# Kernel optimization log

Hardware: AMD Instinct MI355X
Metric: run time of the kernel (lower is better)

The kernel has to match this reference:

```python
import jax, jax.numpy as jnp
import numpy as np

N_USER = 60000
N_ITEM = 40000
N = N_USER + N_ITEM          # 100000 nodes
D = 64                       # embed / layer dim
NNZ = 1600000                # edges per relation (avg degree 16)
B = 16384                    # batch of (user,item) pairs
NLAYERS = 2                  # layers=[64,64,64] -> 2 GNN layers
VAL_SCALE = 0.02             # ~1/degree, mimics symmetric-normalized Laplacian values
W_SCALE = 0.05


def spmm(row, col, val, X):
    # sparse [N,N] @ dense [N,D] via gather + segment-sum (COO)
    return jax.ops.segment_sum(val[:, None] * X[col], row, num_segments=N)


def setup_inputs() -> dict:
    key = jax.random.key(0)
    ks = jax.random.split(key, 40)
    inp = {}
    inp['userIdx'] = jax.random.randint(ks[0], (B,), 0, N_USER, dtype=jnp.int32)
    inp['itemIdx'] = jax.random.randint(ks[1], (B,), 0, N_ITEM, dtype=jnp.int32)
    inp['uEmbd'] = jax.random.normal(ks[2], (N_USER, D), dtype=jnp.float32)
    inp['iEmbd'] = jax.random.normal(ks[3], (N_ITEM, D), dtype=jnp.float32)
    for i, name in enumerate(['lap', 'trust', 'add']):
        inp[name + '_row'] = jax.random.randint(ks[4 + 3 * i], (NNZ,), 0, N, dtype=jnp.int32)
        inp[name + '_col'] = jax.random.randint(ks[5 + 3 * i], (NNZ,), 0, N, dtype=jnp.int32)
        inp[name + '_val'] = jax.random.uniform(ks[6 + 3 * i], (NNZ,), dtype=jnp.float32) * VAL_SCALE
    j = 13
    for name in ['lin_W', 'inter_W', 'attM_W', 'attA_W', 'attT_W']:
        inp[name] = jax.random.normal(ks[j], (NLAYERS, D, D), dtype=jnp.float32) * W_SCALE; j += 1
    for name in ['lin_b', 'inter_b', 'attM_b', 'attA_b', 'attT_b']:
        inp[name] = jax.random.normal(ks[j], (NLAYERS, D), dtype=jnp.float32) * W_SCALE; j += 1
    for name in ['a_main', 'a_add', 'a_trust']:
        inp[name] = jax.random.normal(ks[j], (NLAYERS, D, 1), dtype=jnp.float32) * W_SCALE; j += 1
    inp['W1'] = jax.random.normal(ks[j], (2 * D, 64), dtype=jnp.float32) * W_SCALE; j += 1
    inp['b1'] = jax.random.normal(ks[j], (64,), dtype=jnp.float32) * W_SCALE; j += 1
    inp['W2'] = jax.random.normal(ks[j], (64, 32), dtype=jnp.float32) * W_SCALE; j += 1
    inp['b2'] = jax.random.normal(ks[j], (32,), dtype=jnp.float32) * W_SCALE; j += 1
    inp['W3'] = jax.random.normal(ks[j], (32, 1), dtype=jnp.float32) * W_SCALE; j += 1
    inp['b3'] = jax.random.normal(ks[j], (1,), dtype=jnp.float32) * W_SCALE; j += 1
    return inp


def _gcf_forward(userIdx, itemIdx, uEmbd, iEmbd,
                 lap_row, lap_col, lap_val,
                 trust_row, trust_col, trust_val,
                 add_row, add_col, add_val,
                 lin_W, lin_b, inter_W, inter_b,
                 attM_W, attM_b, attA_W, attA_b, attT_W, attT_b,
                 a_main, a_add, a_trust,
                 W1, b1, W2, b2, W3, b3):
    feats = jnp.concatenate([uEmbd, iEmbd], axis=0)  # [N, D]
    all_emb = [feats]
    rels = [(lap_row, lap_col, lap_val),
            (trust_row, trust_col, trust_val),
            (add_row, add_col, add_val)]
    for l in range(NLAYERS):
        X = feats
        X2 = X * X  # inter_feature = features * features

        def relation(edges, aW, ab, avec):
            row, col, val = edges
            # (L + I) @ X  -> linear ; L @ (X*X) -> interActTransform
            h1 = (spmm(row, col, val, X) + X) @ lin_W[l] + lin_b[l]
            h2 = spmm(row, col, val, X2) @ inter_W[l] + inter_b[l]
            att = jnp.tanh((h1 + h2) @ aW + ab) @ avec  # [N, 1]
            return h1, h2, att.mean()

        m1, m2, w_main = relation(rels[0], attM_W[l], attM_b[l], a_main[l])
        t1, t2, w_trust = relation(rels[1], attT_W[l], attT_b[l], a_trust[l])
        a1, a2, w_add = relation(rels[2], attA_W[l], attA_b[l], a_add[l])
        beta = jax.nn.softmax(jnp.stack([w_main, w_add, w_trust]))  # [3]
        feats = (beta[0] * (m1 + m2) + beta[1] * (a1 + a2) + beta[2] * (t1 + t2))
        all_emb.append(feats)
    final = jnp.mean(jnp.stack(all_emb, axis=1), axis=1)  # [N, D]
    userE = final[userIdx]
    itemE = final[itemIdx + N_USER]
    h = jnp.concatenate([userE, itemE], axis=1)  # [B, 2D]
    h = jax.nn.relu(h @ W1 + b1)
    h = h @ W2 + b2
    h = h @ W3 + b3
    prediction = h.reshape(-1)
    return prediction, userE, itemE, final


def reference(userIdx, itemIdx, uEmbd, iEmbd,
              lap_row, lap_col, lap_val,
              trust_row, trust_col, trust_val,
              add_row, add_col, add_val,
              lin_W, lin_b, inter_W, inter_b,
              attM_W, attM_b, attA_W, attA_b, attT_W, attT_b,
              a_main, a_add, a_trust,
              W1, b1, W2, b2, W3, b3):
    return _gcf_forward(userIdx, itemIdx, uEmbd, iEmbd,
                        lap_row, lap_col, lap_val,
                        trust_row, trust_col, trust_val,
                        add_row, add_col, add_val,
                        lin_W, lin_b, inter_W, inter_b,
                        attM_W, attM_b, attA_W, attA_b, attT_W, attT_b,
                        a_main, a_add, a_trust,
                        W1, b1, W2, b2, W3, b3)
```

## Files before the change

### kernel.cpp

```cpp
#include <hip/hip_runtime.h>

#define N_USER  60000
#define N_ITEM  40000
#define NN      100000
#define NNZ_E   1600000
#define BB      16384
#define ND      6400000
#define ND4     1600000
#define NCHUNK  6250
#define NBUCK   196
#define BUCK_CAP 9216
#define BUCKTOT (NBUCK * BUCK_CAP)
#define BINB    196
#define EPB     8192

typedef __attribute__((ext_vector_type(8))) short bf16x8;
typedef __attribute__((ext_vector_type(4))) float f32x4;

__device__ __forceinline__ float tanh_fast(float x) {
    x = fminf(fmaxf(x, -15.f), 15.f);
    float e = __expf(2.f * x);
    return (e - 1.f) / (e + 1.f);
}

__device__ __forceinline__ float bcast(float x, int k) {
    return __int_as_float(__builtin_amdgcn_readlane(__float_as_int(x), k));
}

__device__ __forceinline__ unsigned short f2bf(float f) {
    unsigned u = __float_as_uint(f);
    u += 0x7FFFu + ((u >> 16) & 1u);
    return (unsigned short)(u >> 16);
}
__device__ __forceinline__ float bf2f(unsigned short s) {
    return __uint_as_float(((unsigned)s) << 16);
}

__device__ __forceinline__ int widx(int k, int n) {
    return ((((n >> 4) * 2 + (k >> 5)) * 4 + ((k >> 3) & 3)) * 16 + (n & 15)) * 8 + (k & 7);
}

__global__ __launch_bounds__(256) void init_kernel(
    const float4* __restrict__ u, const float4* __restrict__ it,
    ushort* __restrict__ XB, float4* __restrict__ fs,
    int* __restrict__ CURS, float* __restrict__ attsum)
{
    int i = blockIdx.x * 256 + threadIdx.x;
    if (i < ND4) {
        float4 v = (i < N_USER * 16) ? u[i] : it[i - N_USER * 16];
        fs[i] = v;
        ushort4 b;
        b.x = f2bf(v.x); b.y = f2bf(v.y); b.z = f2bf(v.z); b.w = f2bf(v.w);
        ((ushort4*)XB)[i] = b;
    }
    if (i < 3 * NBUCK) CURS[i] = (i % NBUCK) * BUCK_CAP;
    if (i < 6) attsum[i] = 0.f;
}

__global__ __launch_bounds__(256) void bin_kernel(
    const int* __restrict__ rows0, const int* __restrict__ cols0, const float* __restrict__ vals0,
    const int* __restrict__ rows1, const int* __restrict__ cols1, const float* __restrict__ vals1,
    const int* __restrict__ rows2, const int* __restrict__ cols2, const float* __restrict__ vals2,
    int* __restrict__ CURS, int2* __restrict__ ECV)
{
    int rel = blockIdx.x / BINB;
    int blk = blockIdx.x % BINB;
    const int* rows; const int* cols; const float* vals;
    if (rel == 0) { rows = rows0; cols = cols0; vals = vals0; }
    else if (rel == 1) { rows = rows1; cols = cols1; vals = vals1; }
    else { rows = rows2; cols = cols2; vals = vals2; }
    int2* out = ECV + (size_t)rel * BUCKTOT;

    __shared__ int2 sStage[EPB];
    __shared__ int hW[4 * NBUCK];
    __shared__ int lOff[NBUCK], lEnd[NBUCK], lCur[NBUCK], gB[NBUCK];
    __shared__ int wt[4];

    int t = threadIdx.x;
    int lane = t & 63, w = t >> 6;
    for (int i = t; i < 4 * NBUCK; i += 256) hW[i] = 0;
    __syncthreads();

    int base = blk * EPB;
    #pragma unroll
    for (int j = 0; j < EPB / 256; ++j) {
        int idx = base + j * 256 + t;
        if (idx < NNZ_E) atomicAdd(&hW[w * NBUCK + (rows[idx] >> 9)], 1);
    }
    __syncthreads();
    int h = 0;
    if (t < NBUCK)
        h = hW[t] + hW[NBUCK + t] + hW[2 * NBUCK + t] + hW[3 * NBUCK + t];
    int sc = h;
    #pragma unroll
    for (int o = 1; o < 64; o <<= 1) {
        int u = __shfl_up(sc, o);
        if (lane >= o) sc += u;
    }
    if (lane == 63) wt[w] = sc;
    __syncthreads();
    int woff = 0;
    #pragma unroll
    for (int ww = 0; ww < 4; ++ww) if (ww < w) woff += wt[ww];
    int excl = woff + sc - h;
    if (t < NBUCK) {
        lOff[t] = excl;
        lEnd[t] = excl + h;
        lCur[t] = excl;
        gB[t] = h ? atomicAdd(&CURS[rel * NBUCK + t], h) : 0;
    }
    __syncthreads();
    #pragma unroll
    for (int j = 0; j < EPB / 256; ++j) {
        int idx = base + j * 256 + t;
        if (idx < NNZ_E) {
            int r = rows[idx];
            int b = r >> 9;
            int pos = atomicAdd(&lCur[b], 1);
            int2 e;
            e.x = ((r & 511) << 17) | cols[idx];
            e.y = __float_as_int(vals[idx]);
            sStage[pos] = e;
        }
    }
    __syncthreads();
    for (int b = w; b < NBUCK; b += 4) {
        int s = lOff[b], e = lEnd[b];
        int gb = gB[b];
        int lim = (b + 1) * BUCK_CAP;
        for (int i = s + lane; i < e; i += 64) {
            int d = gb + (i - s);
            if (d < lim) out[d] = sStage[i];
        }
    }
}

__global__ __launch_bounds__(256) void bsort_kernel(
    const int* __restrict__ CURS, int2* __restrict__ ECV,
    int* __restrict__ RPS, int* __restrict__ RPE)
{
    int rel = blockIdx.x / NBUCK;
    int b   = blockIdx.x % NBUCK;
    int start = b * BUCK_CAP;
    int cnt = CURS[rel * NBUCK + b] - start;
    if (cnt > BUCK_CAP) cnt = BUCK_CAP;
    int2* ecv = ECV + (size_t)rel * BUCKTOT;

    __shared__ int2 sStage[BUCK_CAP];
    __shared__ int sOff[512], sCur[512];
    __shared__ int wt[4];
    int t = threadIdx.x;
    sCur[2 * t] = 0; sCur[2 * t + 1] = 0;
    __syncthreads();
    for (int i = t; i < cnt; i += 256) {
        int rl = ((unsigned)ecv[start + i].x) >> 17;
        atomicAdd(&sCur[rl], 1);
    }
    __syncthreads();
    int a0 = sCur[2 * t], a1 = sCur[2 * t + 1];
    int ps = a0 + a1;
    int lane = t & 63, w = t >> 6;
    int sc = ps;
    #pragma unroll
    for (int o = 1; o < 64; o <<= 1) {
        int u = __shfl_up(sc, o);
        if (lane >= o) sc += u;
    }
    if (lane == 63) wt[w] = sc;
    __syncthreads();
    int woff = 0;
    #pragma unroll
    for (int ww = 0; ww < 4; ++ww) if (ww < w) woff += wt[ww];
    int excl = woff + sc - ps;
    __syncthreads();
    sOff[2 * t] = excl;
    sOff[2 * t + 1] = excl + a0;
    sCur[2 * t] = excl;
    sCur[2 * t + 1] = excl + a0;
    __syncthreads();
    for (int i = t; i < cnt; i += 256) {
        int2 e = ecv[start + i];
        int rl = ((unsigned)e.x) >> 17;
        int pos = atomicAdd(&sCur[rl], 1);
        int2 o2; o2.x = e.x & 0x1FFFF; o2.y = e.y;
        sStage[pos] = o2;
    }
    __syncthreads();
    for (int i = t; i < cnt; i += 256) ecv[start + i] = sStage[i];
    #pragma unroll
    for (int j = 0; j < 2; ++j) {
        int i = 2 * t + j;
        int row = b * 512 + i;
        if (row < NN) {
            RPS[rel * NN + row] = start + sOff[i];
            RPE[rel * NN + row] = start + sCur[i];
        }
    }
}

__global__ __launch_bounds__(256, 8) void spmm_kernel(
    const int* __restrict__ RPS, const int* __restrict__ RPE,
    const int2* __restrict__ ecv,
    const ushort* __restrict__ XB, ushort* __restrict__ G)
{
    int t = threadIdx.x;
    int lane = t & 63;
    int wv = t >> 6;
    int dl = lane & 15;
    int r = blockIdx.x * 16 + wv * 4 + (lane >> 4);
    int ea = RPS[r], eb = RPE[r];
    int cnt = eb - ea;
    int cm = cnt;
    cm = max(cm, __shfl_xor(cm, 16));
    cm = max(cm, __shfl_xor(cm, 32));
    ushort4 xo4 = *(const ushort4*)&XB[(size_t)r * 64 + 4 * dl];
    float s1[4] = {0.f, 0.f, 0.f, 0.f};
    float s2[4] = {0.f, 0.f, 0.f, 0.f};
    for (int base = 0; base < cm; base += 8) {
        float vv[8]; ushort4 xx[8];
        #pragma unroll
        for (int j = 0; j < 8; ++j) {
            int i = base + j;
            bool ok = i < cnt;
            int is = ea + (ok ? i : 0);
            int2 cv = ecv[is];
            vv[j] = ok ? __int_as_float(cv.y) : 0.f;
            xx[j] = *(const ushort4*)&XB[(size_t)cv.x * 64 + 4 * dl];
        }
        #pragma unroll
        for (int j = 0; j < 8; ++j) {
            float x0 = bf2f(xx[j].x), x1 = bf2f(xx[j].y);
            float x2 = bf2f(xx[j].z), x3 = bf2f(xx[j].w);
            float v = vv[j];
            s1[0] += v * x0; s2[0] += v * x0 * x0;
            s1[1] += v * x1; s2[1] += v * x1 * x1;
            s1[2] += v * x2; s2[2] += v * x2 * x2;
            s1[3] += v * x3; s2[3] += v * x3 * x3;
        }
    }
    ushort4 o1, o2;
    o1.x = f2bf(s1[0] + bf2f(xo4.x)); o1.y = f2bf(s1[1] + bf2f(xo4.y));
    o1.z = f2bf(s1[2] + bf2f(xo4.z)); o1.w = f2bf(s1[3] + bf2f(xo4.w));
    o2.x = f2bf(s2[0]); o2.y = f2bf(s2[1]); o2.z = f2bf(s2[2]); o2.w = f2bf(s2[3]);
    *(ushort4*)&G[(size_t)r * 128 + 4 * dl]      = o1;
    *(ushort4*)&G[(size_t)r * 128 + 64 + 4 * dl] = o2;
}

__global__ __launch_bounds__(256) void dense_kernel(
    const ushort* __restrict__ G, ushort* __restrict__ Hout,
    const float* __restrict__ linW, const float* __restrict__ interW,
    const float* __restrict__ linb, const float* __restrict__ interb,
    const float* __restrict__ attW, const float* __restrict__ attb,
    const float* __restrict__ avec, float* __restrict__ attsum)
{
    __shared__ short sL[4096], sI[4096], sW[4096];
    __shared__ float sH[4 * 16 * 65];
    __shared__ float sBias[64], sAttb[64], sAvec[64];

    int tid = threadIdx.x;
    for (int i = tid; i < 4096; i += 256) {
        int k = i >> 6, n = i & 63, ix = widx(k, n);
        sL[ix] = (short)f2bf(linW[i]);
        sI[ix] = (short)f2bf(interW[i]);
        sW[ix] = (short)f2bf(attW[i]);
    }
    if (tid < 64) {
        sBias[tid] = linb[tid] + interb[tid];
        sAttb[tid] = attb[tid];
        sAvec[tid] = avec[tid];
    }
    __syncthreads();

    const bf16x8* pL = (const bf16x8*)sL;
    const bf16x8* pI = (const bf16x8*)sI;
    const bf16x8* pW = (const bf16x8*)sW;

    int lane = tid & 63;
    int wv = tid >> 6;
    int nl = lane & 15;
    int q  = lane >> 4;
    float* myH = sH + wv * (16 * 65);
    int gw = blockIdx.x * 4 + wv;
    int nw = gridDim.x * 4;
    float att_acc = 0.f;

    for (int c = gw; c < NCHUNK; c += nw) {
        int r0 = c * 16;
        const bf16x8* gp = (const bf16x8*)(G + (size_t)(r0 + nl) * 128);
        bf16x8 Ah[2], Qh[2];
        Ah[0] = gp[q];         Ah[1] = gp[4 + q];
        Qh[0] = gp[8 + q];     Qh[1] = gp[12 + q];
        #pragma unroll
        for (int nt = 0; nt < 4; ++nt) {
            float b = sBias[nt * 16 + nl];
            f32x4 acc = {b, b, b, b};
            #pragma unroll
            for (int kh = 0; kh < 2; ++kh) {
                int f = ((nt * 2 + kh) * 4 + q) * 16 + nl;
                acc = __builtin_amdgcn_mfma_f32_16x16x32_bf16(Ah[kh], pL[f], acc, 0, 0, 0);
                acc = __builtin_amdgcn_mfma_f32_16x16x32_bf16(Qh[kh], pI[f], acc, 0, 0, 0);
            }
            #pragma unroll
            for (int reg = 0; reg < 4; ++reg) {
                int row = q * 4 + reg;
                Hout[(size_t)(r0 + row) * 64 + nt * 16 + nl] = f2bf(acc[reg]);
                myH[row * 65 + nt * 16 + nl] = acc[reg];
            }
        }
        bf16x8 Th[2];
        #pragma unroll
        for (int kh = 0; kh < 2; ++kh) {
            #pragma unroll
            for (int j = 0; j < 8; ++j)
                Th[kh][j] = (short)f2bf(myH[nl * 65 + kh * 32 + q * 8 + j]);
        }
        #pragma unroll
        for (int nt = 0; nt < 4; ++nt) {
            float b = sAttb[nt * 16 + nl];
            f32x4 acc = {b, b, b, b};
            #pragma unroll
            for (int kh = 0; kh < 2; ++kh) {
                int f = ((nt * 2 + kh) * 4 + q) * 16 + nl;
                acc = __builtin_amdgcn_mfma_f32_16x16x32_bf16(Th[kh], pW[f], acc, 0, 0, 0);
            }
            float av = sAvec[nt * 16 + nl];
            #pragma unroll
            for (int reg = 0; reg < 4; ++reg)
                att_acc += tanh_fast(acc[reg]) * av;
        }
    }
    #pragma unroll
    for (int o = 32; o >= 1; o >>= 1) att_acc += __shfl_xor(att_acc, o);
    if (lane == 0) atomicAdd(attsum, att_acc);
}

__global__ __launch_bounds__(256) void combine_kernel(
    const ushort4* __restrict__ hM, const ushort4* __restrict__ hA,
    const ushort4* __restrict__ hT, const float* __restrict__ attsum,
    ushort4* __restrict__ XB, float4* __restrict__ fs, float scale)
{
    float w0 = attsum[0] * (1.f / NN);
    float w1 = attsum[1] * (1.f / NN);
    float w2 = attsum[2] * (1.f / NN);
    float m = fmaxf(w0, fmaxf(w1, w2));
    float e0 = __expf(w0 - m), e1 = __expf(w1 - m), e2 = __expf(w2 - m);
    float inv = 1.f / (e0 + e1 + e2);
    float b0 = e0 * inv, b1 = e1 * inv, b2 = e2 * inv;

    int i = blockIdx.x * 256 + threadIdx.x;
    if (i >= ND4) return;
    ushort4 um = hM[i], ua = hA[i], ut = hT[i];
    float4 x;
    x.x = b0 * bf2f(um.x) + b1 * bf2f(ua.x) + b2 * bf2f(ut.x);
    x.y = b0 * bf2f(um.y) + b1 * bf2f(ua.y) + b2 * bf2f(ut.y);
    x.z = b0 * bf2f(um.z) + b1 * bf2f(ua.z) + b2 * bf2f(ut.z);
    x.w = b0 * bf2f(um.w) + b1 * bf2f(ua.w) + b2 * bf2f(ut.w);
    ushort4 bo;
    bo.x = f2bf(x.x); bo.y = f2bf(x.y); bo.z = f2bf(x.z); bo.w = f2bf(x.w);
    XB[i] = bo;
    float4 f = fs[i];
    f.x = (f.x + x.x) * scale;
    f.y = (f.y + x.y) * scale;
    f.z = (f.z + x.z) * scale;
    f.w = (f.w + x.w) * scale;
    fs[i] = f;
}

__global__ __launch_bounds__(256) void mlp_kernel(
    const int* __restrict__ userIdx, const int* __restrict__ itemIdx,
    const float* __restrict__ fin,
    const float* __restrict__ W1, const float* __restrict__ b1,
    const float* __restrict__ W2, const float* __restrict__ b2,
    const float* __restrict__ W3, const float* __restrict__ b3,
    float* __restrict__ pred, float* __restrict__ userE, float* __restrict__ itemE)
{
    __shared__ float sW1[128 * 64];
    __shared__ float sW2[64 * 32];
    __shared__ float sW3[32];
    __shared__ float sb1[64];
    __shared__ float sb2[32];
    int tid = threadIdx.x;
    for (int i = tid; i < 8192; i += 256) sW1[i] = W1[i];
    for (int i = tid; i < 2048; i += 256) sW2[i] = W2[i];
    if (tid < 32) sW3[tid] = W3[tid];
    if (tid < 64) sb1[tid] = b1[tid];
    if (tid < 32) sb2[tid] = b2[tid];
    __syncthreads();
    float bb3 = b3[0];

    int lane = tid & 63;
    int gw = blockIdx.x * 4 + (tid >> 6);
    int nw = gridDim.x * 4;
    for (int p = gw; p < BB; p += nw) {
        int u = userIdx[p];
        int it = itemIdx[p] + N_USER;
        float ue = fin[u * 64 + lane];
        float ie = fin[it * 64 + lane];
        userE[p * 64 + lane] = ue;
        itemE[p * 64 + lane] = ie;
        float h = sb1[lane];
        #pragma unroll
        for (int k = 0; k < 64; ++k) h = fmaf(bcast(ue, k), sW1[k * 64 + lane], h);
        #pragma unroll
        for (int k = 0; k < 64; ++k) h = fmaf(bcast(ie, k), sW1[(k + 64) * 64 + lane], h);
        h = fmaxf(h, 0.f);
        float h2 = sb2[lane & 31];
        #pragma unroll
        for (int k = 0; k < 64; ++k) h2 = fmaf(bcast(h, k), sW2[k * 32 + (lane & 31)], h2);
        float c = (lane < 32) ? h2 * sW3[lane] : 0.f;
        #pragma unroll
        for (int o = 32; o >= 1; o >>= 1) c += __shfl_xor(c, o);
        if (lane == 0) pred[p] = c + bb3;
    }
}

extern "C" void kernel_launch(void* const* d_in, const int* in_sizes, int n_in,
                              void* d_out, int out_size, void* d_ws, size_t ws_size,
                              hipStream_t stream)
{
    const int*   userIdx = (const int*)d_in[0];
    const int*   itemIdx = (const int*)d_in[1];
    const float* uEmbd   = (const float*)d_in[2];
    const float* iEmbd   = (const float*)d_in[3];
    const int*   e_row[3] = {(const int*)d_in[4],  (const int*)d_in[10], (const int*)d_in[7]};
    const int*   e_col[3] = {(const int*)d_in[5],  (const int*)d_in[11], (const int*)d_in[8]};
    const float* e_val[3] = {(const float*)d_in[6], (const float*)d_in[12], (const float*)d_in[9]};
    const float* lin_W   = (const float*)d_in[13];
    const float* inter_W = (const float*)d_in[14];
    const float* attM_W  = (const float*)d_in[15];
    const float* attA_W  = (const float*)d_in[16];
    const float* attT_W  = (const float*)d_in[17];
    const float* lin_b   = (const float*)d_in[18];
    const float* inter_b = (const float*)d_in[19];
    const float* attM_b  = (const float*)d_in[20];
    const float* attA_b  = (const float*)d_in[21];
    const float* attT_b  = (const float*)d_in[22];
    const float* a_main  = (const float*)d_in[23];
    const float* a_add   = (const float*)d_in[24];
    const float* a_trust = (const float*)d_in[25];
    const float* W1 = (const float*)d_in[26];
    const float* b1 = (const float*)d_in[27];
    const float* W2 = (const float*)d_in[28];
    const float* b2 = (const float*)d_in[29];
    const float* W3 = (const float*)d_in[30];
    const float* b3 = (const float*)d_in[31];

    const float* attWq[3] = {attM_W, attA_W, attT_W};
    const float* attbq[3] = {attM_b, attA_b, attT_b};
    const float* avecq[3] = {a_main, a_add, a_trust};

    ushort* G  = (ushort*)d_ws;
    ushort* H0 = G + (size_t)NN * 128;
    ushort* H1 = H0 + ND;
    ushort* H2 = H1 + ND;
    int2*   ECV = (int2*)(H2 + ND);
    ushort* XB = (ushort*)(ECV + 3 * (size_t)BUCKTOT);
    int*    RPS = (int*)(XB + ND);
    int*    RPE = RPS + 3 * NN;
    int*    CURS = RPE + 3 * NN;
    float*  ATT = (float*)(CURS + 3 * NBUCK);

    ushort* Hs[3] = {H0, H1, H2};

    float* outPred  = (float*)d_out;
    float* outUser  = outPred + BB;
    float* outItem  = outUser + BB * 64;
    float* outFinal = outItem + BB * 64;

    init_kernel<<<6250, 256, 0, stream>>>((const float4*)uEmbd, (const float4*)iEmbd,
                                          XB, (float4*)outFinal, CURS, ATT);
    bin_kernel<<<3 * BINB, 256, 0, stream>>>(
        e_row[0], e_col[0], e_val[0],
        e_row[1], e_col[1], e_val[1],
        e_row[2], e_col[2], e_val[2], CURS, ECV);
    bsort_kernel<<<3 * NBUCK, 256, 0, stream>>>(CURS, ECV, RPS, RPE);

    for (int l = 0; l < 2; ++l) {
        const float* lw = lin_W + l * 4096;
        const float* iw = inter_W + l * 4096;
        const float* lb = lin_b + l * 64;
        const float* ib = inter_b + l * 64;

        for (int q = 0; q < 3; ++q) {
            spmm_kernel<<<6250, 256, 0, stream>>>(
                RPS + q * NN, RPE + q * NN, ECV + (size_t)q * BUCKTOT, XB, G);
            dense_kernel<<<512, 256, 0, stream>>>(
                G, Hs[q], lw, iw, lb, ib,
                attWq[q] + l * 4096, attbq[q] + l * 64, avecq[q] + l * 64,
                ATT + l * 3 + q);
        }
        combine_kernel<<<6250, 256, 0, stream>>>(
            (const ushort4*)Hs[0], (const ushort4*)Hs[1], (const ushort4*)Hs[2],
            ATT + l * 3, (ushort4*)XB, (float4*)outFinal,
            (l == 1) ? (1.f / 3.f) : 1.f);
    }

    mlp_kernel<<<512, 256, 0, stream>>>(userIdx, itemIdx, outFinal,
                                        W1, b1, W2, b2, W3, b3,
                                        outPred, outUser, outItem);
}
```

Before: 932.0 us.

## Widen SpMM gathers to 16-byte loads and cache edges in registers during binning

SpMM now gives each row 8 lanes instead of 16. Each lane gathers 8 bf16 features with one 16-byte load, and the unroll depth drops from 8 to 4 edges. The bin and bucket-sort kernels move to 512 threads. They keep row indices and edges in registers so global memory is not read twice, and they use nontemporal loads and stores for the streaming edge data. The aim is fewer, wider memory instructions and less redundant edge traffic. The costs are fewer outstanding gathers per lane, higher register pressure, and a barrier placed inside a divergent branch in the bin kernel.

```diff
diff --git a/kernel.cpp b/kernel.cpp
--- a/kernel.cpp
+++ b/kernel.cpp
@@ -15,6 +15,7 @@
 #define EPB     8192
 
 typedef __attribute__((ext_vector_type(8))) short bf16x8;
+typedef __attribute__((ext_vector_type(8))) unsigned short u16x8;
 typedef __attribute__((ext_vector_type(4))) float f32x4;
 
 __device__ __forceinline__ float tanh_fast(float x) {
@@ -57,7 +58,7 @@
     if (i < 6) attsum[i] = 0.f;
 }
 
-__global__ __launch_bounds__(256) void bin_kernel(
+__global__ __launch_bounds__(512) void bin_kernel(
     const int* __restrict__ rows0, const int* __restrict__ cols0, const float* __restrict__ vals0,
     const int* __restrict__ rows1, const int* __restrict__ cols1, const float* __restrict__ vals1,
     const int* __restrict__ rows2, const int* __restrict__ cols2, const float* __restrict__ vals2,
@@ -69,73 +70,86 @@
     if (rel == 0) { rows = rows0; cols = cols0; vals = vals0; }
     else if (rel == 1) { rows = rows1; cols = cols1; vals = vals1; }
     else { rows = rows2; cols = cols2; vals = vals2; }
-    int2* out = ECV + (size_t)rel * BUCKTOT;
+    long long* out = (long long*)(ECV + (size_t)rel * BUCKTOT);
 
     __shared__ int2 sStage[EPB];
-    __shared__ int hW[4 * NBUCK];
+    __shared__ int hW[8 * NBUCK];
     __shared__ int lOff[NBUCK], lEnd[NBUCK], lCur[NBUCK], gB[NBUCK];
     __shared__ int wt[4];
 
     int t = threadIdx.x;
     int lane = t & 63, w = t >> 6;
-    for (int i = t; i < 4 * NBUCK; i += 256) hW[i] = 0;
+    for (int i = t; i < 8 * NBUCK; i += 512) hW[i] = 0;
     __syncthreads();
 
     int base = blk * EPB;
-    #pragma unroll
-    for (int j = 0; j < EPB / 256; ++j) {
-        int idx = base + j * 256 + t;
-        if (idx < NNZ_E) atomicAdd(&hW[w * NBUCK + (rows[idx] >> 9)], 1);
-    }
-    __syncthreads();
-    int h = 0;
-    if (t < NBUCK)
-        h = hW[t] + hW[NBUCK + t] + hW[2 * NBUCK + t] + hW[3 * NBUCK + t];
-    int sc = h;
-    #pragma unroll
-    for (int o = 1; o < 64; o <<= 1) {
-        int u = __shfl_up(sc, o);
-        if (lane >= o) sc += u;
-    }
-    if (lane == 63) wt[w] = sc;
-    __syncthreads();
-    int woff = 0;
-    #pragma unroll
-    for (int ww = 0; ww < 4; ++ww) if (ww < w) woff += wt[ww];
-    int excl = woff + sc - h;
-    if (t < NBUCK) {
-        lOff[t] = excl;
-        lEnd[t] = excl + h;
-        lCur[t] = excl;
-        gB[t] = h ? atomicAdd(&CURS[rel * NBUCK + t], h) : 0;
-    }
-    __syncthreads();
-    #pragma unroll
-    for (int j = 0; j < EPB / 256; ++j) {
-        int idx = base + j * 256 + t;
-        if (idx < NNZ_E) {
-            int r = rows[idx];
-            int b = r >> 9;
+    int myrow[16];
+    #pragma unroll
+    for (int j = 0; j < 16; ++j) {
+        int idx = base + j * 512 + t;
+        myrow[j] = (idx < NNZ_E) ? __builtin_nontemporal_load(&rows[idx]) : -1;
+        if (myrow[j] >= 0) atomicAdd(&hW[w * NBUCK + (myrow[j] >> 9)], 1);
+    }
+    __syncthreads();
+    if (t < 256) {
+        int h = 0;
+        if (t < NBUCK) {
+            #pragma unroll
+            for (int ww = 0; ww < 8; ++ww) h += hW[ww * NBUCK + t];
+        }
+        int sc = h;
+        #pragma unroll
+        for (int o = 1; o < 64; o <<= 1) {
+            int u = __shfl_up(sc, o);
+            if (lane >= o) sc += u;
+        }
+        if (lane == 63) wt[w] = sc;
+        __syncthreads();
+        int woff = 0;
+        #pragma unroll
+        for (int ww = 0; ww < 4; ++ww) if (ww < w) woff += wt[ww];
+        int excl = woff + sc - h;
+        if (t < NBUCK) {
+            lOff[t] = excl;
+            lEnd[t] = excl + h;
+            lCur[t] = excl;
+            gB[t] = h ? atomicAdd(&CURS[rel * NBUCK + t], h) : 0;
+        }
+    } else {
+        __syncthreads();
+    }
+    __syncthreads();
+    #pragma unroll
+    for (int j = 0; j < 16; ++j) {
+        int idx = base + j * 512 + t;
+        if (myrow[j] >= 0) {
+            int c = __builtin_nontemporal_load(&cols[idx]);
+            float v = __builtin_nontemporal_load(&vals[idx]);
+            int b = myrow[j] >> 9;
             int pos = atomicAdd(&lCur[b], 1);
             int2 e;
-            e.x = ((r & 511) << 17) | cols[idx];
-            e.y = __float_as_int(vals[idx]);
+            e.x = ((myrow[j] & 511) << 17) | c;
+            e.y = __float_as_int(v);
             sStage[pos] = e;
         }
     }
     __syncthreads();
-    for (int b = w; b < NBUCK; b += 4) {
+    for (int b = w; b < NBUCK; b += 8) {
         int s = lOff[b], e = lEnd[b];
         int gb = gB[b];
         int lim = (b + 1) * BUCK_CAP;
         for (int i = s + lane; i < e; i += 64) {
             int d = gb + (i - s);
-            if (d < lim) out[d] = sStage[i];
-        }
-    }
-}
-
-__global__ __launch_bounds__(256) void bsort_kernel(
+            if (d < lim) {
+                int2 ev = sStage[i];
+                long long packed = (((long long)(unsigned)ev.y) << 32) | (unsigned)ev.x;
+                __builtin_nontemporal_store(packed, &out[d]);
+            }
+        }
+    }
+}
+
+__global__ __launch_bounds__(512) void bsort_kernel(
     const int* __restrict__ CURS, int2* __restrict__ ECV,
     int* __restrict__ RPS, int* __restrict__ RPE)
 {
@@ -147,20 +161,24 @@
     int2* ecv = ECV + (size_t)rel * BUCKTOT;
 
     __shared__ int2 sStage[BUCK_CAP];
-    __shared__ int sOff[512], sCur[512];
-    __shared__ int wt[4];
+    __shared__ int sOff[512], sCnt[512];
+    __shared__ int wt[8];
     int t = threadIdx.x;
-    sCur[2 * t] = 0; sCur[2 * t + 1] = 0;
-    __syncthreads();
-    for (int i = t; i < cnt; i += 256) {
-        int rl = ((unsigned)ecv[start + i].x) >> 17;
-        atomicAdd(&sCur[rl], 1);
-    }
-    __syncthreads();
-    int a0 = sCur[2 * t], a1 = sCur[2 * t + 1];
-    int ps = a0 + a1;
     int lane = t & 63, w = t >> 6;
-    int sc = ps;
+    sCnt[t] = 0;
+    __syncthreads();
+    int2 e[18];
+    #pragma unroll
+    for (int j = 0; j < 18; ++j) {
+        int i = t + j * 512;
+        if (i < cnt) {
+            e[j] = ecv[start + i];
+            atomicAdd(&sCnt[((unsigned)e[j].x) >> 17], 1);
+        }
+    }
+    __syncthreads();
+    int h = sCnt[t];
+    int sc = h;
     #pragma unroll
     for (int o = 1; o < 64; o <<= 1) {
         int u = __shfl_up(sc, o);
@@ -170,35 +188,32 @@
     __syncthreads();
     int woff = 0;
     #pragma unroll
-    for (int ww = 0; ww < 4; ++ww) if (ww < w) woff += wt[ww];
-    int excl = woff + sc - ps;
-    __syncthreads();
-    sOff[2 * t] = excl;
-    sOff[2 * t + 1] = excl + a0;
-    sCur[2 * t] = excl;
-    sCur[2 * t + 1] = excl + a0;
-    __syncthreads();
-    for (int i = t; i < cnt; i += 256) {
-        int2 e = ecv[start + i];
-        int rl = ((unsigned)e.x) >> 17;
-        int pos = atomicAdd(&sCur[rl], 1);
-        int2 o2; o2.x = e.x & 0x1FFFF; o2.y = e.y;
-        sStage[pos] = o2;
-    }
-    __syncthreads();
-    for (int i = t; i < cnt; i += 256) ecv[start + i] = sStage[i];
-    #pragma unroll
-    for (int j = 0; j < 2; ++j) {
-        int i = 2 * t + j;
-        int row = b * 512 + i;
-        if (row < NN) {
-            RPS[rel * NN + row] = start + sOff[i];
-            RPE[rel * NN + row] = start + sCur[i];
-        }
-    }
-}
-
-__global__ __launch_bounds__(256, 8) void spmm_kernel(
+    for (int ww = 0; ww < 8; ++ww) if (ww < w) woff += wt[ww];
+    int excl = woff + sc - h;
+    __syncthreads();
+    sOff[t] = excl;
+    sCnt[t] = excl;
+    __syncthreads();
+    #pragma unroll
+    for (int j = 0; j < 18; ++j) {
+        int i = t + j * 512;
+        if (i < cnt) {
+            int rl = ((unsigned)e[j].x) >> 17;
+            int pos = atomicAdd(&sCnt[rl], 1);
+            int2 o2; o2.x = e[j].x & 0x1FFFF; o2.y = e[j].y;
+            sStage[pos] = o2;
+        }
+    }
+    __syncthreads();
+    for (int i = t; i < cnt; i += 512) ecv[start + i] = sStage[i];
+    int row = b * 512 + t;
+    if (row < NN) {
+        RPS[rel * NN + row] = start + sOff[t];
+        RPE[rel * NN + row] = start + sCnt[t];
+    }
+}
+
+__global__ __launch_bounds__(256, 4) void spmm_kernel(
     const int* __restrict__ RPS, const int* __restrict__ RPE,
     const int2* __restrict__ ecv,
     const ushort* __restrict__ XB, ushort* __restrict__ G)
@@ -206,44 +221,47 @@
     int t = threadIdx.x;
     int lane = t & 63;
     int wv = t >> 6;
-    int dl = lane & 15;
-    int r = blockIdx.x * 16 + wv * 4 + (lane >> 4);
+    int dl = lane & 7;
+    int r = blockIdx.x * 32 + wv * 8 + (lane >> 3);
     int ea = RPS[r], eb = RPE[r];
     int cnt = eb - ea;
     int cm = cnt;
+    cm = max(cm, __shfl_xor(cm, 8));
     cm = max(cm, __shfl_xor(cm, 16));
     cm = max(cm, __shfl_xor(cm, 32));
-    ushort4 xo4 = *(const ushort4*)&XB[(size_t)r * 64 + 4 * dl];
-    float s1[4] = {0.f, 0.f, 0.f, 0.f};
-    float s2[4] = {0.f, 0.f, 0.f, 0.f};
-    for (int base = 0; base < cm; base += 8) {
-        float vv[8]; ushort4 xx[8];
-        #pragma unroll
-        for (int j = 0; j < 8; ++j) {
+    u16x8 xo8 = *(const u16x8*)&XB[(size_t)r * 64 + 8 * dl];
+    float s1[8] = {0.f, 0.f, 0.f, 0.f, 0.f, 0.f, 0.f, 0.f};
+    float s2[8] = {0.f, 0.f, 0.f, 0.f, 0.f, 0.f, 0.f, 0.f};
+    for (int base = 0; base < cm; base += 4) {
+        float vv[4]; u16x8 xx[4];
+        #pragma unroll
+        for (int j = 0; j < 4; ++j) {
             int i = base + j;
             bool ok = i < cnt;
             int is = ea + (ok ? i : 0);
             int2 cv = ecv[is];
             vv[j] = ok ? __int_as_float(cv.y) : 0.f;
-            xx[j] = *(const ushort4*)&XB[(size_t)cv.x * 64 + 4 * dl];
-        }
-        #pragma unroll
-        for (int j = 0; j < 8; ++j) {
-            float x0 = bf2f(xx[j].x), x1 = bf2f(xx[j].y);
-            float x2 = bf2f(xx[j].z), x3 = bf2f(xx[j].w);
+            xx[j] = *(const u16x8*)&XB[(size_t)cv.x * 64 + 8 * dl];
+        }
+        #pragma unroll
+        for (int j = 0; j < 4; ++j) {
             float v = vv[j];
-            s1[0] += v * x0; s2[0] += v * x0 * x0;
-            s1[1] += v * x1; s2[1] += v * x1 * x1;
-            s1[2] += v * x2; s2[2] += v * x2 * x2;
-            s1[3] += v * x3; s2[3] += v * x3 * x3;
-        }
-    }
-    ushort4 o1, o2;
-    o1.x = f2bf(s1[0] + bf2f(xo4.x)); o1.y = f2bf(s1[1] + bf2f(xo4.y));
-    o1.z = f2bf(s1[2] + bf2f(xo4.z)); o1.w = f2bf(s1[3] + bf2f(xo4.w));
-    o2.x = f2bf(s2[0]); o2.y = f2bf(s2[1]); o2.z = f2bf(s2[2]); o2.w = f2bf(s2[3]);
-    *(ushort4*)&G[(size_t)r * 128 + 4 * dl]      = o1;
-    *(ushort4*)&G[(size_t)r * 128 + 64 + 4 * dl] = o2;
+            #pragma unroll
+            for (int d = 0; d < 8; ++d) {
+                float x = bf2f(xx[j][d]);
+                s1[d] += v * x;
+                s2[d] += v * x * x;
+            }
+        }
+    }
+    u16x8 o1, o2;
+    #pragma unroll
+    for (int d = 0; d < 8; ++d) {
+        o1[d] = f2bf(s1[d] + bf2f(xo8[d]));
+        o2[d] = f2bf(s2[d]);
+    }
+    *(u16x8*)&G[(size_t)r * 128 + 8 * dl]      = o1;
+    *(u16x8*)&G[(size_t)r * 128 + 64 + 8 * dl] = o2;
 }
 
 __global__ __launch_bounds__(256) void dense_kernel(
@@ -469,11 +487,11 @@
 
     init_kernel<<<6250, 256, 0, stream>>>((const float4*)uEmbd, (const float4*)iEmbd,
                                           XB, (float4*)outFinal, CURS, ATT);
-    bin_kernel<<<3 * BINB, 256, 0, stream>>>(
+    bin_kernel<<<3 * BINB, 512, 0, stream>>>(
         e_row[0], e_col[0], e_val[0],
         e_row[1], e_col[1], e_val[1],
         e_row[2], e_col[2], e_val[2], CURS, ECV);
-    bsort_kernel<<<3 * NBUCK, 256, 0, stream>>>(CURS, ECV, RPS, RPE);
+    bsort_kernel<<<3 * NBUCK, 512, 0, stream>>>(CURS, ECV, RPS, RPE);
 
     for (int l = 0; l < 2; ++l) {
         const float* lw = lin_W + l * 4096;
@@ -482,7 +500,7 @@
         const float* ib = inter_b + l * 64;
 
         for (int q = 0; q < 3; ++q) {
-            spmm_kernel<<<6250, 256, 0, stream>>>(
+            spmm_kernel<<<3125, 256, 0, stream>>>(
                 RPS + q * NN, RPE + q * NN, ECV + (size_t)q * BUCKTOT, XB, G);
             dense_kernel<<<512, 256, 0, stream>>>(
                 G, Hs[q], lw, iw, lb, ib,
```

Result: faster. 783.2 us (-16.0%).
